# Kernel tuning notes

Measured on AMD Instinct MI355X. Metric: run time of the kernel, lower is better.

Reference implementation:

```python
import jax, jax.numpy as jnp
import numpy as np
import math

NUM_FREQS = 16  # module init num_freqs


def posenc(x, nf):
    # x [..., D] -> [..., D*2*nf]
    freqs = 2.0 ** jnp.arange(nf, dtype=x.dtype)
    xf = x[..., None] * freqs  # [..., D, nf]
    enc = jnp.concatenate([jnp.sin(xf), jnp.cos(xf)], axis=-1)  # [..., D, 2nf]
    return enc.reshape(x.shape[:-1] + (x.shape[-1] * 2 * nf,))


def plucker(rays):
    # rays [..., 6] = [origin, direction] -> [d_norm, cross(o, d_norm)]
    o, dv = rays[..., :3], rays[..., 3:]
    dn = dv / (jnp.linalg.norm(dv, axis=-1, keepdims=True) + 1e-8)
    return jnp.concatenate([dn, jnp.cross(o, dn)], axis=-1)


def grid_sample_bilinear(img, grid):
    # img [N,C,H,W], grid [N,Hg,Wg,2] in [-1,1], align_corners=True, zeros padding
    N, C, H, W = img.shape
    x = (grid[..., 0] + 1.0) * 0.5 * (W - 1)
    y = (grid[..., 1] + 1.0) * 0.5 * (H - 1)
    x0 = jnp.floor(x); x1 = x0 + 1.0
    y0 = jnp.floor(y); y1 = y0 + 1.0
    wx1 = x - x0; wx0 = 1.0 - wx1
    wy1 = y - y0; wy0 = 1.0 - wy1

    def gather(ix, iy):
        valid = ((ix >= 0) & (ix <= W - 1) & (iy >= 0) & (iy <= H - 1)).astype(img.dtype)
        ixc = jnp.clip(ix, 0, W - 1).astype(jnp.int32)
        iyc = jnp.clip(iy, 0, H - 1).astype(jnp.int32)
        vals = jax.vmap(lambda im, iyn, ixn: im[:, iyn, ixn])(img, iyc, ixc)  # [N,C,Hg,Wg]
        return vals * valid[:, None]

    return (gather(x0, y0) * (wx0 * wy0)[:, None]
            + gather(x1, y0) * (wx1 * wy0)[:, None]
            + gather(x0, y1) * (wx0 * wy1)[:, None]
            + gather(x1, y1) * (wx1 * wy1)[:, None])


def _forward(xref, mask_ref, ray_points, rays, R, T, focal, W1, b1, W2, b2, Wv, bv, Wd):
    F = NUM_FREQS
    b, n, hw, c = xref.shape
    d = ray_points.shape[3]
    res = int(math.sqrt(hw))
    # mask (already at res x res; nearest resize is identity)
    xref = xref * mask_ref.reshape(b, n, hw, 1)
    # project sample points into all n+1 camera NDC frames
    pts = ray_points[:, 0]  # [b,hw,d,3]
    p_view = jnp.einsum('bhdk,bvkj->bvhdj', pts, R) + T[:, :, None, None]  # [b,n+1,hw,d,3]
    ndc = focal[:, :, None, None, None] * p_view[..., :2] / p_view[..., 2:3]
    grid = jax.lax.stop_gradient(jnp.clip(jnp.nan_to_num(-ndc[:, 1:]), -1.2, 1.2))
    grid = grid.reshape(b * n, hw, d, 2)
    img = xref.reshape(b * n, res, res, c).transpose(0, 3, 1, 2)  # [(bn),c,res,res]
    pf = grid_sample_bilinear(img, grid)  # [(bn),c,hw,d]
    plane_features = pf.reshape(b, n, c, hw, d).transpose(0, 1, 3, 4, 2)  # [b,n,hw,d,c]

    xyz_iv = p_view                       # view-space points [b,n+1,hw,d,3]
    xyz_iv_enc = posenc(xyz_iv, F)        # [b,n+1,hw,d,6F]

    # target rays (view 0) expressed in every view frame
    o_t, d_t = rays[:, 0, :, :3], rays[:, 0, :, 3:]
    o_iv = jnp.einsum('bhk,bvkj->bvhj', o_t, R) + T[:, :, None]
    d_iv = jnp.einsum('bhk,bvkj->bvhj', d_t, R)
    cam_iv = jnp.concatenate([o_iv, d_iv], -1)[:, 1:]  # [b,n,hw,6]
    cam_iv = jnp.broadcast_to(cam_iv[:, :, :, None, :], (b, n, hw, d, 6))
    cam_iv_enc = posenc(plucker(cam_iv), F // 2)  # [b,n,hw,d,6F]

    xyz_grid = jnp.broadcast_to(xyz_iv_enc[:, :1], (b, n, hw, d, xyz_iv_enc.shape[-1]))
    # reference-view ray origins in target frame
    o_r = rays[:, 1:, :, :3]
    o_tg = jnp.einsum('bnhk,bkj->bnhj', o_r, R[:, 0]) + T[:, 0][:, None, None]
    cam_feat = jnp.broadcast_to(o_tg[:, :, :, None, :], (b, n, hw, d, 3))
    cam_feat_enc = posenc(cam_feat, F)

    plane_in = jnp.concatenate([plane_features, xyz_iv_enc[:, 1:], xyz_iv[:, 1:],
                                cam_iv_enc, cam_iv[..., 3:]], axis=-1)  # [b,n,hw,d,326]
    h = jax.nn.silu(plane_in @ W1 + b1)
    pf_final = h @ W2 + b2  # [b,n,hw,d,C]

    attn_in = jnp.concatenate([plane_features, xyz_grid,
                               jnp.broadcast_to(xyz_iv[:, :1], (b, n, hw, d, 3)),
                               cam_feat, cam_feat_enc], axis=-1)  # [b,n,hw,d,326]
    attn = jax.nn.softmax(attn_in @ Wv + bv, axis=1)  # softmax over views
    fused = (pf_final * attn).sum(1)  # [b,hw,d,C]
    out = fused @ Wd  # decoder (no bias) -> [b,hw,d,1]
    return jnp.concatenate([fused, out], axis=-1), attn


def setup_inputs() -> dict:
    B, N, RES, D, C = 1, 4, 32, 32, 128
    HW = RES * RES
    IN_DIM = C + NUM_FREQS * 3 * 4 + 6  # 326
    key = jax.random.key(0)
    ks = jax.random.split(key, 16)
    xref = jax.random.normal(ks[0], (B, N, HW, C), jnp.float32)
    mask_ref = (jax.random.uniform(ks[1], (B, N, RES, RES)) > 0.1).astype(jnp.float32)
    ray_points = jax.random.uniform(ks[2], (B, 1, HW, D, 3), minval=-0.5, maxval=0.5)
    o = jax.random.uniform(ks[3], (B, N + 1, HW, 3), minval=-0.2, maxval=0.2)
    dirs = jax.random.normal(ks[4], (B, N + 1, HW, 3))
    dirs = dirs / jnp.linalg.norm(dirs, axis=-1, keepdims=True)
    rays = jnp.concatenate([o, dirs], -1)
    R = jnp.linalg.qr(jax.random.normal(ks[5], (B, N + 1, 3, 3)))[0]
    T = jnp.concatenate([jax.random.uniform(ks[6], (B, N + 1, 2), minval=-0.2, maxval=0.2),
                         jax.random.uniform(ks[7], (B, N + 1, 1), minval=2.0, maxval=2.5)], -1)
    focal = jax.random.uniform(ks[8], (B, N + 1), minval=0.8, maxval=1.2)
    W1 = jax.random.normal(ks[9], (IN_DIM, C)) / np.sqrt(IN_DIM)
    b1 = jnp.zeros((C,), jnp.float32)
    W2 = jax.random.normal(ks[10], (C, C)) / np.sqrt(C)
    b2 = jnp.zeros((C,), jnp.float32)
    Wv = jax.random.normal(ks[11], (IN_DIM, 1)) / np.sqrt(IN_DIM)
    bv = jnp.zeros((1,), jnp.float32)
    Wd = jax.random.normal(ks[12], (C, 1)) * 0.01  # zero_module in source; small random for meaningful baseline
    return {"xref": xref, "mask_ref": mask_ref, "ray_points": ray_points, "rays": rays,
            "R": R, "T": T, "focal": focal, "W1": W1, "b1": b1, "W2": W2, "b2": b2,
            "Wv": Wv, "bv": bv, "Wd": Wd}


def reference(xref, mask_ref, ray_points, rays, R, T, focal, W1, b1, W2, b2, Wv, bv, Wd):
    return _forward(xref, mask_ref, ray_points, rays, R, T, focal, W1, b1, W2, b2, Wv, bv, Wd)
```

## Files before the change

### kernel.cpp

```cpp
#include <hip/hip_runtime.h>
#include <hip/hip_bf16.h>
#include <math.h>

#define XH 1024
#define XD 32
#define XC 128
#define XK 326

typedef __attribute__((ext_vector_type(8))) short bf16x8;
typedef __attribute__((ext_vector_type(4))) float f32x4;

__device__ __forceinline__ unsigned short f2b(float f) {
  unsigned u = __float_as_uint(f);
  return (unsigned short)((u + 0x7FFFu + ((u >> 16) & 1u)) >> 16);
}
__device__ __forceinline__ float b2f(unsigned short b) {
  return __uint_as_float(((unsigned)b) << 16);
}
__device__ __forceinline__ unsigned pk2bf(float v0, float v1) {
  __hip_bfloat162 h = __float22bfloat162_rn(make_float2(v0, v1));
  return *reinterpret_cast<unsigned*>(&h);
}

#define WT1 (12 * 8 * 64)
#define WT2 (4 * 8 * 64)

__global__ void prep_frags(const float* __restrict__ W1,
                           const float* __restrict__ W2,
                           unsigned int* __restrict__ ws) {
  int f = blockIdx.x * 256 + threadIdx.x;
  if (f >= WT1 + WT2) return;
  const float* W; int KMAX; int fl; size_t hoff, loff;
  if (f < WT1) { W = W1; KMAX = XK; fl = f; hoff = 0; loff = WT1; }
  else { W = W2; KMAX = XC; fl = f - WT1; hoff = 2 * (size_t)WT1; loff = 2 * (size_t)WT1 + WT2; }
  int l = fl & 63, ct = (fl >> 6) & 7, kc = fl >> 9;
  int c = ct * 16 + (l & 15);
  int kbase = kc * 32 + 8 * (l >> 4);
  unsigned hi[4], lo[4];
  #pragma unroll
  for (int jj = 0; jj < 4; ++jj) {
    int k0 = kbase + 2 * jj;
    float w0 = (k0     < KMAX) ? W[k0 * XC + c]       : 0.f;
    float w1 = (k0 + 1 < KMAX) ? W[(k0 + 1) * XC + c] : 0.f;
    unsigned short h0 = f2b(w0); unsigned short l0 = f2b(w0 - b2f(h0));
    unsigned short h1 = f2b(w1); unsigned short l1 = f2b(w1 - b2f(h1));
    hi[jj] = (unsigned)h0 | ((unsigned)h1 << 16);
    lo[jj] = (unsigned)l0 | ((unsigned)l1 << 16);
  }
  uint4 vh; vh.x = hi[0]; vh.y = hi[1]; vh.z = hi[2]; vh.w = hi[3];
  uint4 vl; vl.x = lo[0]; vl.y = lo[1]; vl.z = lo[2]; vl.w = lo[3];
  *(uint4*)(ws + (hoff + fl) * 4) = vh;
  *(uint4*)(ws + (loff + fl) * 4) = vl;
}


__global__ __launch_bounds__(512, 4)
void nerf_main(const float* __restrict__ xref,
               const float* __restrict__ mask,
               const float* __restrict__ rpts,
               const float* __restrict__ rays,
               const float* __restrict__ Rm,
               const float* __restrict__ Tm,
               const float* __restrict__ focp,
               const float* __restrict__ b1p,
               const float* __restrict__ b2p,
               const float* __restrict__ Wvp,
               const float* __restrict__ bvp,
               const float* __restrict__ Wdp,
               const bf16x8* __restrict__ wfrag,
               float* __restrict__ out0,
               float* __restrict__ out1)
{
  const int h = blockIdx.x;
  const int tid = threadIdx.x;

  __shared__ float sR[5][3][3];
  __shared__ float sT[5][3];
  __shared__ float sFoc[5];
  __shared__ float sRay[5][6];
  __shared__ float sOiv[5][3];
  __shared__ float sDiv[5][3];
  __shared__ float sPlk[4][6];
  __shared__ float sOtg[4][3];
  __shared__ float sPv[5][32][3];
  __shared__ float sBc[4][32][4];
  __shared__ int   sBp[4][32][4];
  __shared__ float sWv[XK];
  __shared__ float sAt[32];
  __shared__ float sBt[4];
  __shared__ float sLogit[4][32];
  __shared__ float sAw[4][32];
  __shared__ float sOutPart[4][32];
  __shared__ __align__(16) unsigned short sEnc2[4][128];
  __shared__ __align__(16) unsigned char uMem[65536];
  unsigned short* sFcHi = (unsigned short*)uMem;
  unsigned short* sFcLo = (unsigned short*)(uMem + 32768);
  unsigned short* sHbHi = (unsigned short*)(uMem + 32768);
  unsigned short* sHbLo = sHbHi + 32 * 128;
  float*          sOut  = (float*)uMem;

  for (int i = tid; i < 45; i += 512) ((float*)sR)[i] = Rm[i];
  for (int i = tid; i < 15; i += 512) ((float*)sT)[i] = Tm[i];
  for (int i = tid; i < 5;  i += 512) sFoc[i] = focp[i];
  for (int i = tid; i < 30; i += 512) { int v = i / 6, j = i % 6; sRay[v][j] = rays[(v*XH + h)*6 + j]; }
  for (int i = tid; i < XK; i += 512) sWv[i] = Wvp[i];
  __syncthreads();

  if (tid < 160) {
    int v = tid >> 5, d = tid & 31;
    float p0 = rpts[(h*XD + d)*3 + 0];
    float p1 = rpts[(h*XD + d)*3 + 1];
    float p2 = rpts[(h*XD + d)*3 + 2];
    #pragma unroll
    for (int j = 0; j < 3; ++j)
      sPv[v][d][j] = p0*sR[v][0][j] + p1*sR[v][1][j] + p2*sR[v][2][j] + sT[v][j];
  } else if (tid < 165) {
    int v = tid - 160;
    #pragma unroll
    for (int j = 0; j < 3; ++j) {
      sOiv[v][j] = sRay[0][0]*sR[v][0][j] + sRay[0][1]*sR[v][1][j] + sRay[0][2]*sR[v][2][j] + sT[v][j];
      sDiv[v][j] = sRay[0][3]*sR[v][0][j] + sRay[0][4]*sR[v][1][j] + sRay[0][5]*sR[v][2][j];
    }
  }
  __syncthreads();

  if (tid < 4) {
    int n = tid;
    float d0 = sDiv[n+1][0], d1 = sDiv[n+1][1], d2 = sDiv[n+1][2];
    float inv = 1.f / (sqrtf(d0*d0 + d1*d1 + d2*d2) + 1e-8f);
    float n0 = d0*inv, n1 = d1*inv, n2 = d2*inv;
    float o0 = sOiv[n+1][0], o1 = sOiv[n+1][1], o2 = sOiv[n+1][2];
    sPlk[n][0] = n0; sPlk[n][1] = n1; sPlk[n][2] = n2;
    sPlk[n][3] = o1*n2 - o2*n1;
    sPlk[n][4] = o2*n0 - o0*n2;
    sPlk[n][5] = o0*n1 - o1*n0;
    #pragma unroll
    for (int j = 0; j < 3; ++j)
      sOtg[n][j] = sRay[1+n][0]*sR[0][0][j] + sRay[1+n][1]*sR[0][1][j] + sRay[1+n][2]*sR[0][2][j] + sT[0][j];
  }
  if (tid >= 32 && tid < 160) {
    int idx = tid - 32, n = idx >> 5, d = idx & 31, v = n + 1;
    float px = sPv[v][d][0], py = sPv[v][d][1], pz = sPv[v][d][2], fo = sFoc[v];
    float gx = -(fo*px)/pz, gy = -(fo*py)/pz;
    if (isnan(gx)) gx = 0.f;
    if (isnan(gy)) gy = 0.f;
    gx = fminf(fmaxf(gx, -1.2f), 1.2f);
    gy = fminf(fmaxf(gy, -1.2f), 1.2f);
    float x = (gx + 1.f)*15.5f, y = (gy + 1.f)*15.5f;
    float x0f = floorf(x), y0f = floorf(y);
    float wx1 = x - x0f, wx0 = 1.f - wx1;
    float wy1 = y - y0f, wy0 = 1.f - wy1;
    int x0i = (int)x0f, y0i = (int)y0f;
    bool vx0 = (x0f >=  0.f) & (x0f <= 31.f);
    bool vx1 = (x0f >= -1.f) & (x0f <= 30.f);
    bool vy0 = (y0f >=  0.f) & (y0f <= 31.f);
    bool vy1 = (y0f >= -1.f) & (y0f <= 30.f);
    int x0c = min(max(x0i, 0), 31), x1c = min(max(x0i + 1, 0), 31);
    int y0c = min(max(y0i, 0), 31), y1c = min(max(y0i + 1, 0), 31);
    int p00 = y0c*32 + x0c, p10 = y0c*32 + x1c, p01 = y1c*32 + x0c, p11 = y1c*32 + x1c;
    sBc[n][d][0] = wx0*wy0*((vx0 && vy0) ? mask[n*XH + p00] : 0.f);
    sBc[n][d][1] = wx1*wy0*((vx1 && vy0) ? mask[n*XH + p10] : 0.f);
    sBc[n][d][2] = wx0*wy1*((vx0 && vy1) ? mask[n*XH + p01] : 0.f);
    sBc[n][d][3] = wx1*wy1*((vx1 && vy1) ? mask[n*XH + p11] : 0.f);
    sBp[n][d][0] = p00; sBp[n][d][1] = p10; sBp[n][d][2] = p01; sBp[n][d][3] = p11;
  }
  if (tid >= 256) {
    int t = tid - 256;
    int d = t >> 3, sub = t & 7;
    float p = 0.f;
    for (int kk = sub * 12; kk < sub * 12 + 12; ++kk) {
      int comp = kk >> 5, idx = kk & 31;
      float ang = sPv[0][d][comp] * (float)(1 << (idx & 15));
      float ev = (idx < 16) ? __sinf(ang) : __cosf(ang);
      p += ev * sWv[128 + kk];
    }
    if (sub == 0)
      for (int j = 0; j < 3; ++j) p += sPv[0][d][j] * sWv[224 + j];
    #pragma unroll
    for (int o = 1; o < 8; o <<= 1) p += __shfl_xor(p, o);
    if (sub == 0) sAt[d] = p;
  }
  __syncthreads();

  {
    int n = tid >> 7, off = tid & 127;
    float val = 0.f;
    if (off >= 3 && off < 99) {
      int kk = off - 3;
      int comp = kk >> 4, idx = kk & 15;
      float ang = sPlk[n][comp] * (float)(1 << (idx & 7));
      val = (idx < 8) ? __sinf(ang) : __cosf(ang);
    } else if (off >= 99 && off < 102) {
      val = sDiv[n + 1][off - 99];
    }
    sEnc2[n][off] = f2b(val);
  }
  if (tid >= 256 && tid < 288) {
    int t = tid - 256, n = t >> 3, sub = t & 7;
    float p = 0.f;
    for (int kk = sub * 12; kk < sub * 12 + 12; ++kk) {
      int comp = kk >> 5, idx = kk & 31;
      float ang = sOtg[n][comp] * (float)(1 << (idx & 15));
      float ev = (idx < 16) ? __sinf(ang) : __cosf(ang);
      p += ev * sWv[230 + kk];
    }
    if (sub == 0) {
      for (int j = 0; j < 3; ++j) p += sOtg[n][j] * sWv[227 + j];
      p += bvp[0];
    }
    #pragma unroll
    for (int o = 1; o < 8; o <<= 1) p += __shfl_xor(p, o);
    if (sub == 0) sBt[n] = p;
  }
  __syncthreads();

  const int brow = tid >> 2;
  const int bn = brow & 3, bd = brow >> 2;
  const int kloc0 = (tid & 3) * 16;
  float plog = 0.f;

  {
    const float* bc = sBc[bn][bd];
    const int*   bp = sBp[bn][bd];
    const float* xb = xref + bn * XH * XC;
    #pragma unroll
    for (int chunk = 0; chunk < 2; ++chunk) {
      int kg = chunk * 64 + kloc0;
      float vv[16];
      #pragma unroll
      for (int q = 0; q < 4; ++q) {
        float4 a0 = *(const float4*)(xb + bp[0] * XC + kg + 4 * q);
        float4 a1 = *(const float4*)(xb + bp[1] * XC + kg + 4 * q);
        float4 a2 = *(const float4*)(xb + bp[2] * XC + kg + 4 * q);
        float4 a3 = *(const float4*)(xb + bp[3] * XC + kg + 4 * q);
        #pragma unroll
        for (int j = 0; j < 4; ++j)
          vv[4 * q + j] = bc[0]*(&a0.x)[j] + bc[1]*(&a1.x)[j]
                        + bc[2]*(&a2.x)[j] + bc[3]*(&a3.x)[j];
      }
      #pragma unroll
      for (int j = 0; j < 16; ++j) plog += vv[j] * sWv[kg + j];
      #pragma unroll
      for (int q = 0; q < 2; ++q) {
        unsigned ph[4], pl[4];
        #pragma unroll
        for (int j = 0; j < 4; ++j) {
          float v0 = vv[8 * q + 2 * j], v1 = vv[8 * q + 2 * j + 1];
          unsigned hp = pk2bf(v0, v1);
          float r0 = v0 - b2f((unsigned short)(hp & 0xFFFF));
          float r1 = v1 - b2f((unsigned short)(hp >> 16));
          ph[j] = hp;
          pl[j] = pk2bf(r0, r1);
        }
        int gidx = (brow * 128 + kg + 8 * q) ^ ((brow & 7) << 3);
        *(uint4*)&sFcHi[gidx] = *(uint4*)ph;
        *(uint4*)&sFcLo[gidx] = *(uint4*)pl;
      }
    }
    {
      float p = plog;
      p += __shfl_xor(p, 1);
      p += __shfl_xor(p, 2);
      if ((tid & 3) == 0) sLogit[bn][bd] = p;
    }
  }
  __syncthreads();

  if (tid < 32) {
    int d = tid;
    float l0 = sLogit[0][d] + sAt[d] + sBt[0];
    float l1 = sLogit[1][d] + sAt[d] + sBt[1];
    float l2 = sLogit[2][d] + sAt[d] + sBt[2];
    float l3 = sLogit[3][d] + sAt[d] + sBt[3];
    float m = fmaxf(fmaxf(l0, l1), fmaxf(l2, l3));
    float e0 = __expf(l0 - m), e1 = __expf(l1 - m), e2 = __expf(l2 - m), e3 = __expf(l3 - m);
    float inv = 1.f / (e0 + e1 + e2 + e3);
    float w0 = e0*inv, w1 = e1*inv, w2 = e2*inv, w3 = e3*inv;
    sAw[0][d] = w0; sAw[1][d] = w1; sAw[2][d] = w2; sAw[3][d] = w3;
    out1[(0*XH + h)*XD + d] = w0;
    out1[(1*XH + h)*XD + d] = w1;
    out1[(2*XH + h)*XD + d] = w2;
    out1[(3*XH + h)*XD + d] = w3;
  }

  const int w = tid >> 6, lane = tid & 63;
  const int rt = w & 3, cg = w >> 2;
  const int lrow = lane & 15, lg = lane >> 4;
  float bias1[4];
  #pragma unroll
  for (int ct = 0; ct < 4; ++ct) bias1[ct] = b1p[cg * 64 + ct * 16 + lrow];

  f32x4 acc1[2][4];
  #pragma unroll
  for (int rf = 0; rf < 2; ++rf)
    #pragma unroll
    for (int ct = 0; ct < 4; ++ct) acc1[rf][ct] = (f32x4){0.f, 0.f, 0.f, 0.f};

  #pragma unroll
  for (int sk = 0; sk < 4; ++sk) {
    const int r0 = rt * 32 + lrow;
    const int ai0 = (r0 * 128 + sk * 32 + 8 * lg) ^ ((r0 & 7) << 3);
    const int ai1 = ai0 + 16 * 128;
    bf16x8 ah0 = *(const bf16x8*)&sFcHi[ai0];
    bf16x8 ah1 = *(const bf16x8*)&sFcHi[ai1];
    bf16x8 al0 = *(const bf16x8*)&sFcLo[ai0];
    bf16x8 al1 = *(const bf16x8*)&sFcLo[ai1];
    const bf16x8* wkh = wfrag + (sk * 8 + cg * 4) * 64 + lane;
    const bf16x8* wkl = wkh + WT1;
    #pragma unroll
    for (int ct = 0; ct < 4; ++ct) {
      bf16x8 bh = wkh[ct * 64];
      bf16x8 bl = wkl[ct * 64];
      acc1[0][ct] = __builtin_amdgcn_mfma_f32_16x16x32_bf16(ah0, bh, acc1[0][ct], 0, 0, 0);
      acc1[0][ct] = __builtin_amdgcn_mfma_f32_16x16x32_bf16(ah0, bl, acc1[0][ct], 0, 0, 0);
      acc1[0][ct] = __builtin_amdgcn_mfma_f32_16x16x32_bf16(al0, bh, acc1[0][ct], 0, 0, 0);
      acc1[1][ct] = __builtin_amdgcn_mfma_f32_16x16x32_bf16(ah1, bh, acc1[1][ct], 0, 0, 0);
      acc1[1][ct] = __builtin_amdgcn_mfma_f32_16x16x32_bf16(ah1, bl, acc1[1][ct], 0, 0, 0);
      acc1[1][ct] = __builtin_amdgcn_mfma_f32_16x16x32_bf16(al1, bh, acc1[1][ct], 0, 0, 0);
    }
  }

  {
    const int r0c = rt * 32 + lrow;
    const int nn = r0c & 3;
    const int dd = r0c >> 2;
    const float* pv0 = sPv[nn + 1][dd];
    const float* pv1 = sPv[nn + 1][dd + 4];
    const unsigned short* enc = sEnc2[nn];
    const float m0 = (lg & 1) ? 256.f : 1.f;
    const bool usn = (lg < 2);

    auto mfma4 = [&](int kc, bf16x8 A0, bf16x8 A1) {
      const bf16x8* wkh = wfrag + (kc * 8 + cg * 4) * 64 + lane;
      const bf16x8* wkl = wkh + WT1;
      #pragma unroll
      for (int ct = 0; ct < 4; ++ct) {
        bf16x8 bh = wkh[ct * 64];
        bf16x8 bl = wkl[ct * 64];
        acc1[0][ct] = __builtin_amdgcn_mfma_f32_16x16x32_bf16(A0, bh, acc1[0][ct], 0, 0, 0);
        acc1[0][ct] = __builtin_amdgcn_mfma_f32_16x16x32_bf16(A0, bl, acc1[0][ct], 0, 0, 0);
        acc1[1][ct] = __builtin_amdgcn_mfma_f32_16x16x32_bf16(A1, bh, acc1[1][ct], 0, 0, 0);
        acc1[1][ct] = __builtin_amdgcn_mfma_f32_16x16x32_bf16(A1, bl, acc1[1][ct], 0, 0, 0);
      }
    };
    auto trigf = [&](const float* pv, int comp) -> bf16x8 {
      float pA = pv[comp] * m0;
      unsigned ph[4];
      #pragma unroll
      for (int mj = 0; mj < 4; ++mj) {
        float a0f = pA * (float)(1 << (2 * mj));
        float a1f = pA * (float)(1 << (2 * mj + 1));
        float v0 = usn ? __sinf(a0f) : __cosf(a0f);
        float v1 = usn ? __sinf(a1f) : __cosf(a1f);
        ph[mj] = pk2bf(v0, v1);
      }
      union { unsigned u[4]; bf16x8 f; } cv;
      cv.u[0] = ph[0]; cv.u[1] = ph[1]; cv.u[2] = ph[2]; cv.u[3] = ph[3];
      return cv.f;
    };
    auto encf = [&](int off) -> bf16x8 {
      return *(const bf16x8*)&enc[off + lg * 8];
    };

    mfma4(4, trigf(pv0, 0), trigf(pv1, 0));
    mfma4(5, trigf(pv0, 1), trigf(pv1, 1));
    mfma4(6, trigf(pv0, 2), trigf(pv1, 2));
    {
      bf16x8 e0 = encf(0);
      bf16x8 e1 = e0;
      if (lg == 0) {
        e0[0] = (short)f2b(pv0[0]); e0[1] = (short)f2b(pv0[1]); e0[2] = (short)f2b(pv0[2]);
        e1[0] = (short)f2b(pv1[0]); e1[1] = (short)f2b(pv1[1]); e1[2] = (short)f2b(pv1[2]);
      }
      mfma4(7, e0, e1);
    }
    { bf16x8 e = encf(32); mfma4(8, e, e); }
    { bf16x8 e = encf(64); mfma4(9, e, e); }
    { bf16x8 e = encf(96); mfma4(10, e, e); }
  }
  __syncthreads();

  #pragma unroll
  for (int rf = 0; rf < 2; ++rf) {
    int d = (rt * 2 + rf) * 4 + lg;
    float a0 = sAw[0][d], a1 = sAw[1][d], a2 = sAw[2][d], a3 = sAw[3][d];
    #pragma unroll
    for (int ct = 0; ct < 4; ++ct) {
      int c = cg * 64 + ct * 16 + lrow;
      float x0 = acc1[rf][ct][0] + bias1[ct];
      float x1 = acc1[rf][ct][1] + bias1[ct];
      float x2 = acc1[rf][ct][2] + bias1[ct];
      float x3 = acc1[rf][ct][3] + bias1[ct];
      float hb = a0 * __fdividef(x0, 1.f + __expf(-x0))
               + a1 * __fdividef(x1, 1.f + __expf(-x1))
               + a2 * __fdividef(x2, 1.f + __expf(-x2))
               + a3 * __fdividef(x3, 1.f + __expf(-x3));
      unsigned short hh = f2b(hb);
      unsigned short hl = f2b(hb - b2f(hh));
      int idx = (d * 128 + c) ^ ((d & 7) << 3);
      sHbHi[idx] = hh; sHbLo[idx] = hl;
    }
  }
  __syncthreads();

  const int rt2 = w & 1, cg2 = w >> 1;
  float bias2[2], wdv[2];
  #pragma unroll
  for (int cti = 0; cti < 2; ++cti) {
    int c = cg2 * 32 + cti * 16 + lrow;
    bias2[cti] = b2p[c]; wdv[cti] = Wdp[c];
  }
  f32x4 acc2[2];
  acc2[0] = (f32x4){0.f, 0.f, 0.f, 0.f};
  acc2[1] = (f32x4){0.f, 0.f, 0.f, 0.f};
  {
    const int ar = rt2 * 16 + lrow;
    #pragma unroll
    for (int kc = 0; kc < 4; ++kc) {
      int aidx = (ar * 128 + kc * 32 + 8 * lg) ^ ((ar & 7) << 3);
      bf16x8 ah = *(const bf16x8*)&sHbHi[aidx];
      bf16x8 al = *(const bf16x8*)&sHbLo[aidx];
      const bf16x8* wkh = wfrag + 2 * WT1 + (kc * 8 + cg2 * 2) * 64 + lane;
      const bf16x8* wkl = wkh + WT2;
      #pragma unroll
      for (int cti = 0; cti < 2; ++cti) {
        bf16x8 bh = wkh[cti * 64];
        bf16x8 bl = wkl[cti * 64];
        acc2[cti] = __builtin_amdgcn_mfma_f32_16x16x32_bf16(ah, bh, acc2[cti], 0, 0, 0);
        acc2[cti] = __builtin_amdgcn_mfma_f32_16x16x32_bf16(ah, bl, acc2[cti], 0, 0, 0);
        acc2[cti] = __builtin_amdgcn_mfma_f32_16x16x32_bf16(al, bh, acc2[cti], 0, 0, 0);
      }
    }
  }

  {
    float part[4] = {0.f, 0.f, 0.f, 0.f};
    #pragma unroll
    for (int cti = 0; cti < 2; ++cti) {
      int c = cg2 * 32 + cti * 16 + lrow;
      #pragma unroll
      for (int i = 0; i < 4; ++i) {
        int d = rt2 * 16 + lg * 4 + i;
        float fv = acc2[cti][i] + bias2[cti];
        sOut[d * 129 + c] = fv;
        part[i] += fv * wdv[cti];
      }
    }
    #pragma unroll
    for (int i = 0; i < 4; ++i) {
      float p = part[i];
      #pragma unroll
      for (int o = 1; o < 16; o <<= 1) p += __shfl_xor(p, o);
      if (lrow == 0) sOutPart[cg2][rt2 * 16 + lg * 4 + i] = p;
    }
  }
  __syncthreads();
  if (tid < 32)
    sOut[tid * 129 + 128] =
      sOutPart[0][tid] + sOutPart[1][tid] + sOutPart[2][tid] + sOutPart[3][tid];
  __syncthreads();
  {
    const float4* src = (const float4*)sOut;
    float4* dst = (float4*)(out0 + (size_t)h * (XD * 129));
    for (int i = tid; i < (XD * 129) / 4; i += 512) dst[i] = src[i];
  }
}

extern "C" void kernel_launch(void* const* d_in, const int* in_sizes, int n_in,
                              void* d_out, int out_size, void* d_ws, size_t ws_size,
                              hipStream_t stream) {
  const float* xref = (const float*)d_in[0];
  const float* mask = (const float*)d_in[1];
  const float* rpts = (const float*)d_in[2];
  const float* rays = (const float*)d_in[3];
  const float* Rm   = (const float*)d_in[4];
  const float* Tm   = (const float*)d_in[5];
  const float* foc  = (const float*)d_in[6];
  const float* W1   = (const float*)d_in[7];
  const float* b1   = (const float*)d_in[8];
  const float* W2   = (const float*)d_in[9];
  const float* b2   = (const float*)d_in[10];
  const float* Wv   = (const float*)d_in[11];
  const float* bv   = (const float*)d_in[12];
  const float* Wd   = (const float*)d_in[13];
  float* out0 = (float*)d_out;
  float* out1 = out0 + (size_t)XH * XD * 129;

  hipLaunchKernelGGL(prep_frags, dim3(32), dim3(256), 0, stream,
                     W1, W2, (unsigned int*)d_ws);
  hipLaunchKernelGGL(nerf_main, dim3(XH), dim3(512), 0, stream,
                     xref, mask, rpts, rays, Rm, Tm, foc,
                     b1, b2, Wv, bv, Wd, (const bf16x8*)d_ws, out0, out1);
}
```

Baseline: 71.63 us.

## Split each ray across two 256-thread blocks handling 16 depth samples each

The main kernel now launches twice as many blocks of 256 threads, each processing half of the 32 depth samples for one ray. Shared memory use per block roughly halves and the MFMA tiling is reorganised so each wave owns 16 rows and all 128 output columns. The aim is better occupancy and finer load balancing across CUs. In exchange, per-ray setup work (camera transforms, Plucker encodings, target attention terms) is duplicated in both blocks, and each wave reads the full weight fragment set.

```diff
diff --git a/kernel.cpp b/kernel.cpp
--- a/kernel.cpp
+++ b/kernel.cpp
@@ -54,7 +54,7 @@
 }
 
 
-__global__ __launch_bounds__(512, 4)
+__global__ __launch_bounds__(256, 4)
 void nerf_main(const float* __restrict__ xref,
                const float* __restrict__ mask,
                const float* __restrict__ rpts,
@@ -71,7 +71,8 @@
                float* __restrict__ out0,
                float* __restrict__ out1)
 {
-  const int h = blockIdx.x;
+  const int h = blockIdx.x >> 1;
+  const int q = blockIdx.x & 1;
   const int tid = threadIdx.x;
 
   __shared__ float sR[5][3][3];
@@ -82,40 +83,40 @@
   __shared__ float sDiv[5][3];
   __shared__ float sPlk[4][6];
   __shared__ float sOtg[4][3];
-  __shared__ float sPv[5][32][3];
-  __shared__ float sBc[4][32][4];
-  __shared__ int   sBp[4][32][4];
+  __shared__ float sPv[5][16][3];
+  __shared__ float sBc[4][16][4];
+  __shared__ int   sBp[4][16][4];
   __shared__ float sWv[XK];
-  __shared__ float sAt[32];
+  __shared__ float sAt[16];
   __shared__ float sBt[4];
-  __shared__ float sLogit[4][32];
-  __shared__ float sAw[4][32];
-  __shared__ float sOutPart[4][32];
+  __shared__ float sLogit[4][16];
+  __shared__ float sAw[4][16];
+  __shared__ float sOutPart[4][16];
   __shared__ __align__(16) unsigned short sEnc2[4][128];
-  __shared__ __align__(16) unsigned char uMem[65536];
+  __shared__ __align__(16) unsigned char uMem[32768];
   unsigned short* sFcHi = (unsigned short*)uMem;
-  unsigned short* sFcLo = (unsigned short*)(uMem + 32768);
-  unsigned short* sHbHi = (unsigned short*)(uMem + 32768);
-  unsigned short* sHbLo = sHbHi + 32 * 128;
+  unsigned short* sFcLo = (unsigned short*)(uMem + 16384);
+  unsigned short* sHbHi = (unsigned short*)(uMem + 16384);
+  unsigned short* sHbLo = sHbHi + 16 * 128;
   float*          sOut  = (float*)uMem;
 
-  for (int i = tid; i < 45; i += 512) ((float*)sR)[i] = Rm[i];
-  for (int i = tid; i < 15; i += 512) ((float*)sT)[i] = Tm[i];
-  for (int i = tid; i < 5;  i += 512) sFoc[i] = focp[i];
-  for (int i = tid; i < 30; i += 512) { int v = i / 6, j = i % 6; sRay[v][j] = rays[(v*XH + h)*6 + j]; }
-  for (int i = tid; i < XK; i += 512) sWv[i] = Wvp[i];
-  __syncthreads();
-
-  if (tid < 160) {
-    int v = tid >> 5, d = tid & 31;
+  for (int i = tid; i < 45; i += 256) ((float*)sR)[i] = Rm[i];
+  for (int i = tid; i < 15; i += 256) ((float*)sT)[i] = Tm[i];
+  for (int i = tid; i < 5;  i += 256) sFoc[i] = focp[i];
+  for (int i = tid; i < 30; i += 256) { int v = i / 6, j = i % 6; sRay[v][j] = rays[(v*XH + h)*6 + j]; }
+  for (int i = tid; i < XK; i += 256) sWv[i] = Wvp[i];
+  __syncthreads();
+
+  if (tid < 80) {
+    int v = tid >> 4, ld = tid & 15, d = q * 16 + ld;
     float p0 = rpts[(h*XD + d)*3 + 0];
     float p1 = rpts[(h*XD + d)*3 + 1];
     float p2 = rpts[(h*XD + d)*3 + 2];
     #pragma unroll
     for (int j = 0; j < 3; ++j)
-      sPv[v][d][j] = p0*sR[v][0][j] + p1*sR[v][1][j] + p2*sR[v][2][j] + sT[v][j];
-  } else if (tid < 165) {
-    int v = tid - 160;
+      sPv[v][ld][j] = p0*sR[v][0][j] + p1*sR[v][1][j] + p2*sR[v][2][j] + sT[v][j];
+  } else if (tid < 85) {
+    int v = tid - 80;
     #pragma unroll
     for (int j = 0; j < 3; ++j) {
       sOiv[v][j] = sRay[0][0]*sR[v][0][j] + sRay[0][1]*sR[v][1][j] + sRay[0][2]*sR[v][2][j] + sT[v][j];
@@ -138,9 +139,9 @@
     for (int j = 0; j < 3; ++j)
       sOtg[n][j] = sRay[1+n][0]*sR[0][0][j] + sRay[1+n][1]*sR[0][1][j] + sRay[1+n][2]*sR[0][2][j] + sT[0][j];
   }
-  if (tid >= 32 && tid < 160) {
-    int idx = tid - 32, n = idx >> 5, d = idx & 31, v = n + 1;
-    float px = sPv[v][d][0], py = sPv[v][d][1], pz = sPv[v][d][2], fo = sFoc[v];
+  if (tid >= 32 && tid < 96) {
+    int idx = tid - 32, n = idx >> 4, ld = idx & 15, v = n + 1;
+    float px = sPv[v][ld][0], py = sPv[v][ld][1], pz = sPv[v][ld][2], fo = sFoc[v];
     float gx = -(fo*px)/pz, gy = -(fo*py)/pz;
     if (isnan(gx)) gx = 0.f;
     if (isnan(gy)) gy = 0.f;
@@ -158,32 +159,32 @@
     int x0c = min(max(x0i, 0), 31), x1c = min(max(x0i + 1, 0), 31);
     int y0c = min(max(y0i, 0), 31), y1c = min(max(y0i + 1, 0), 31);
     int p00 = y0c*32 + x0c, p10 = y0c*32 + x1c, p01 = y1c*32 + x0c, p11 = y1c*32 + x1c;
-    sBc[n][d][0] = wx0*wy0*((vx0 && vy0) ? mask[n*XH + p00] : 0.f);
-    sBc[n][d][1] = wx1*wy0*((vx1 && vy0) ? mask[n*XH + p10] : 0.f);
-    sBc[n][d][2] = wx0*wy1*((vx0 && vy1) ? mask[n*XH + p01] : 0.f);
-    sBc[n][d][3] = wx1*wy1*((vx1 && vy1) ? mask[n*XH + p11] : 0.f);
-    sBp[n][d][0] = p00; sBp[n][d][1] = p10; sBp[n][d][2] = p01; sBp[n][d][3] = p11;
-  }
-  if (tid >= 256) {
-    int t = tid - 256;
-    int d = t >> 3, sub = t & 7;
+    sBc[n][ld][0] = wx0*wy0*((vx0 && vy0) ? mask[n*XH + p00] : 0.f);
+    sBc[n][ld][1] = wx1*wy0*((vx1 && vy0) ? mask[n*XH + p10] : 0.f);
+    sBc[n][ld][2] = wx0*wy1*((vx0 && vy1) ? mask[n*XH + p01] : 0.f);
+    sBc[n][ld][3] = wx1*wy1*((vx1 && vy1) ? mask[n*XH + p11] : 0.f);
+    sBp[n][ld][0] = p00; sBp[n][ld][1] = p10; sBp[n][ld][2] = p01; sBp[n][ld][3] = p11;
+  }
+  if (tid >= 128) {
+    int t = tid - 128;
+    int ld = t >> 3, sub = t & 7;
     float p = 0.f;
     for (int kk = sub * 12; kk < sub * 12 + 12; ++kk) {
       int comp = kk >> 5, idx = kk & 31;
-      float ang = sPv[0][d][comp] * (float)(1 << (idx & 15));
+      float ang = sPv[0][ld][comp] * (float)(1 << (idx & 15));
       float ev = (idx < 16) ? __sinf(ang) : __cosf(ang);
       p += ev * sWv[128 + kk];
     }
     if (sub == 0)
-      for (int j = 0; j < 3; ++j) p += sPv[0][d][j] * sWv[224 + j];
+      for (int j = 0; j < 3; ++j) p += sPv[0][ld][j] * sWv[224 + j];
     #pragma unroll
     for (int o = 1; o < 8; o <<= 1) p += __shfl_xor(p, o);
-    if (sub == 0) sAt[d] = p;
-  }
-  __syncthreads();
-
-  {
-    int n = tid >> 7, off = tid & 127;
+    if (sub == 0) sAt[ld] = p;
+  }
+  __syncthreads();
+
+  for (int s = tid; s < 512; s += 256) {
+    int n = s >> 7, off = s & 127;
     float val = 0.f;
     if (off >= 3 && off < 99) {
       int kk = off - 3;
@@ -195,8 +196,8 @@
     }
     sEnc2[n][off] = f2b(val);
   }
-  if (tid >= 256 && tid < 288) {
-    int t = tid - 256, n = t >> 3, sub = t & 7;
+  if (tid >= 224) {
+    int t = tid - 224, n = t >> 3, sub = t & 7;
     float p = 0.f;
     for (int kk = sub * 12; kk < sub * 12 + 12; ++kk) {
       int comp = kk >> 5, idx = kk & 31;
@@ -215,44 +216,44 @@
   __syncthreads();
 
   const int brow = tid >> 2;
-  const int bn = brow & 3, bd = brow >> 2;
+  const int bn = brow & 3, bld = brow >> 2;
   const int kloc0 = (tid & 3) * 16;
   float plog = 0.f;
 
   {
-    const float* bc = sBc[bn][bd];
-    const int*   bp = sBp[bn][bd];
+    const float* bc = sBc[bn][bld];
+    const int*   bp = sBp[bn][bld];
     const float* xb = xref + bn * XH * XC;
     #pragma unroll
     for (int chunk = 0; chunk < 2; ++chunk) {
       int kg = chunk * 64 + kloc0;
       float vv[16];
       #pragma unroll
-      for (int q = 0; q < 4; ++q) {
-        float4 a0 = *(const float4*)(xb + bp[0] * XC + kg + 4 * q);
-        float4 a1 = *(const float4*)(xb + bp[1] * XC + kg + 4 * q);
-        float4 a2 = *(const float4*)(xb + bp[2] * XC + kg + 4 * q);
-        float4 a3 = *(const float4*)(xb + bp[3] * XC + kg + 4 * q);
+      for (int qq = 0; qq < 4; ++qq) {
+        float4 a0 = *(const float4*)(xb + bp[0] * XC + kg + 4 * qq);
+        float4 a1 = *(const float4*)(xb + bp[1] * XC + kg + 4 * qq);
+        float4 a2 = *(const float4*)(xb + bp[2] * XC + kg + 4 * qq);
+        float4 a3 = *(const float4*)(xb + bp[3] * XC + kg + 4 * qq);
         #pragma unroll
         for (int j = 0; j < 4; ++j)
-          vv[4 * q + j] = bc[0]*(&a0.x)[j] + bc[1]*(&a1.x)[j]
-                        + bc[2]*(&a2.x)[j] + bc[3]*(&a3.x)[j];
+          vv[4 * qq + j] = bc[0]*(&a0.x)[j] + bc[1]*(&a1.x)[j]
+                         + bc[2]*(&a2.x)[j] + bc[3]*(&a3.x)[j];
       }
       #pragma unroll
       for (int j = 0; j < 16; ++j) plog += vv[j] * sWv[kg + j];
       #pragma unroll
-      for (int q = 0; q < 2; ++q) {
+      for (int qq = 0; qq < 2; ++qq) {
         unsigned ph[4], pl[4];
         #pragma unroll
         for (int j = 0; j < 4; ++j) {
-          float v0 = vv[8 * q + 2 * j], v1 = vv[8 * q + 2 * j + 1];
+          float v0 = vv[8 * qq + 2 * j], v1 = vv[8 * qq + 2 * j + 1];
           unsigned hp = pk2bf(v0, v1);
           float r0 = v0 - b2f((unsigned short)(hp & 0xFFFF));
           float r1 = v1 - b2f((unsigned short)(hp >> 16));
           ph[j] = hp;
           pl[j] = pk2bf(r0, r1);
         }
-        int gidx = (brow * 128 + kg + 8 * q) ^ ((brow & 7) << 3);
+        int gidx = (brow * 128 + kg + 8 * qq) ^ ((brow & 7) << 3);
         *(uint4*)&sFcHi[gidx] = *(uint4*)ph;
         *(uint4*)&sFcLo[gidx] = *(uint4*)pl;
       }
@@ -261,22 +262,22 @@
       float p = plog;
       p += __shfl_xor(p, 1);
       p += __shfl_xor(p, 2);
-      if ((tid & 3) == 0) sLogit[bn][bd] = p;
-    }
-  }
-  __syncthreads();
-
-  if (tid < 32) {
-    int d = tid;
-    float l0 = sLogit[0][d] + sAt[d] + sBt[0];
-    float l1 = sLogit[1][d] + sAt[d] + sBt[1];
-    float l2 = sLogit[2][d] + sAt[d] + sBt[2];
-    float l3 = sLogit[3][d] + sAt[d] + sBt[3];
+      if ((tid & 3) == 0) sLogit[bn][bld] = p;
+    }
+  }
+  __syncthreads();
+
+  if (tid < 16) {
+    int ld = tid, d = q * 16 + ld;
+    float l0 = sLogit[0][ld] + sAt[ld] + sBt[0];
+    float l1 = sLogit[1][ld] + sAt[ld] + sBt[1];
+    float l2 = sLogit[2][ld] + sAt[ld] + sBt[2];
+    float l3 = sLogit[3][ld] + sAt[ld] + sBt[3];
     float m = fmaxf(fmaxf(l0, l1), fmaxf(l2, l3));
     float e0 = __expf(l0 - m), e1 = __expf(l1 - m), e2 = __expf(l2 - m), e3 = __expf(l3 - m);
     float inv = 1.f / (e0 + e1 + e2 + e3);
     float w0 = e0*inv, w1 = e1*inv, w2 = e2*inv, w3 = e3*inv;
-    sAw[0][d] = w0; sAw[1][d] = w1; sAw[2][d] = w2; sAw[3][d] = w3;
+    sAw[0][ld] = w0; sAw[1][ld] = w1; sAw[2][ld] = w2; sAw[3][ld] = w3;
     out1[(0*XH + h)*XD + d] = w0;
     out1[(1*XH + h)*XD + d] = w1;
     out1[(2*XH + h)*XD + d] = w2;
@@ -284,63 +285,49 @@
   }
 
   const int w = tid >> 6, lane = tid & 63;
-  const int rt = w & 3, cg = w >> 2;
   const int lrow = lane & 15, lg = lane >> 4;
-  float bias1[4];
+  float bias1[8];
   #pragma unroll
-  for (int ct = 0; ct < 4; ++ct) bias1[ct] = b1p[cg * 64 + ct * 16 + lrow];
-
-  f32x4 acc1[2][4];
+  for (int ct = 0; ct < 8; ++ct) bias1[ct] = b1p[ct * 16 + lrow];
+
+  f32x4 acc1[8];
   #pragma unroll
-  for (int rf = 0; rf < 2; ++rf)
-    #pragma unroll
-    for (int ct = 0; ct < 4; ++ct) acc1[rf][ct] = (f32x4){0.f, 0.f, 0.f, 0.f};
+  for (int ct = 0; ct < 8; ++ct) acc1[ct] = (f32x4){0.f, 0.f, 0.f, 0.f};
 
   #pragma unroll
   for (int sk = 0; sk < 4; ++sk) {
-    const int r0 = rt * 32 + lrow;
+    const int r0 = w * 16 + lrow;
     const int ai0 = (r0 * 128 + sk * 32 + 8 * lg) ^ ((r0 & 7) << 3);
-    const int ai1 = ai0 + 16 * 128;
-    bf16x8 ah0 = *(const bf16x8*)&sFcHi[ai0];
-    bf16x8 ah1 = *(const bf16x8*)&sFcHi[ai1];
-    bf16x8 al0 = *(const bf16x8*)&sFcLo[ai0];
-    bf16x8 al1 = *(const bf16x8*)&sFcLo[ai1];
-    const bf16x8* wkh = wfrag + (sk * 8 + cg * 4) * 64 + lane;
-    const bf16x8* wkl = wkh + WT1;
-    #pragma unroll
-    for (int ct = 0; ct < 4; ++ct) {
-      bf16x8 bh = wkh[ct * 64];
-      bf16x8 bl = wkl[ct * 64];
-      acc1[0][ct] = __builtin_amdgcn_mfma_f32_16x16x32_bf16(ah0, bh, acc1[0][ct], 0, 0, 0);
-      acc1[0][ct] = __builtin_amdgcn_mfma_f32_16x16x32_bf16(ah0, bl, acc1[0][ct], 0, 0, 0);
-      acc1[0][ct] = __builtin_amdgcn_mfma_f32_16x16x32_bf16(al0, bh, acc1[0][ct], 0, 0, 0);
-      acc1[1][ct] = __builtin_amdgcn_mfma_f32_16x16x32_bf16(ah1, bh, acc1[1][ct], 0, 0, 0);
-      acc1[1][ct] = __builtin_amdgcn_mfma_f32_16x16x32_bf16(ah1, bl, acc1[1][ct], 0, 0, 0);
-      acc1[1][ct] = __builtin_amdgcn_mfma_f32_16x16x32_bf16(al1, bh, acc1[1][ct], 0, 0, 0);
-    }
-  }
-
-  {
-    const int r0c = rt * 32 + lrow;
+    bf16x8 ah = *(const bf16x8*)&sFcHi[ai0];
+    bf16x8 al = *(const bf16x8*)&sFcLo[ai0];
+    const bf16x8* wk = wfrag + (sk * 8) * 64 + lane;
+    #pragma unroll
+    for (int ct = 0; ct < 8; ++ct) {
+      bf16x8 bh = wk[ct * 64];
+      bf16x8 bl = wk[WT1 + ct * 64];
+      acc1[ct] = __builtin_amdgcn_mfma_f32_16x16x32_bf16(ah, bh, acc1[ct], 0, 0, 0);
+      acc1[ct] = __builtin_amdgcn_mfma_f32_16x16x32_bf16(ah, bl, acc1[ct], 0, 0, 0);
+      acc1[ct] = __builtin_amdgcn_mfma_f32_16x16x32_bf16(al, bh, acc1[ct], 0, 0, 0);
+    }
+  }
+
+  {
+    const int r0c = w * 16 + lrow;
     const int nn = r0c & 3;
     const int dd = r0c >> 2;
     const float* pv0 = sPv[nn + 1][dd];
-    const float* pv1 = sPv[nn + 1][dd + 4];
     const unsigned short* enc = sEnc2[nn];
     const float m0 = (lg & 1) ? 256.f : 1.f;
     const bool usn = (lg < 2);
 
-    auto mfma4 = [&](int kc, bf16x8 A0, bf16x8 A1) {
-      const bf16x8* wkh = wfrag + (kc * 8 + cg * 4) * 64 + lane;
-      const bf16x8* wkl = wkh + WT1;
-      #pragma unroll
-      for (int ct = 0; ct < 4; ++ct) {
-        bf16x8 bh = wkh[ct * 64];
-        bf16x8 bl = wkl[ct * 64];
-        acc1[0][ct] = __builtin_amdgcn_mfma_f32_16x16x32_bf16(A0, bh, acc1[0][ct], 0, 0, 0);
-        acc1[0][ct] = __builtin_amdgcn_mfma_f32_16x16x32_bf16(A0, bl, acc1[0][ct], 0, 0, 0);
-        acc1[1][ct] = __builtin_amdgcn_mfma_f32_16x16x32_bf16(A1, bh, acc1[1][ct], 0, 0, 0);
-        acc1[1][ct] = __builtin_amdgcn_mfma_f32_16x16x32_bf16(A1, bl, acc1[1][ct], 0, 0, 0);
+    auto mfmaB = [&](int kc, bf16x8 A0) {
+      const bf16x8* wk = wfrag + (kc * 8) * 64 + lane;
+      #pragma unroll
+      for (int ct = 0; ct < 8; ++ct) {
+        bf16x8 bh = wk[ct * 64];
+        bf16x8 bl = wk[WT1 + ct * 64];
+        acc1[ct] = __builtin_amdgcn_mfma_f32_16x16x32_bf16(A0, bh, acc1[ct], 0, 0, 0);
+        acc1[ct] = __builtin_amdgcn_mfma_f32_16x16x32_bf16(A0, bl, acc1[ct], 0, 0, 0);
       }
     };
     auto trigf = [&](const float* pv, int comp) -> bf16x8 {
@@ -362,70 +349,65 @@
       return *(const bf16x8*)&enc[off + lg * 8];
     };
 
-    mfma4(4, trigf(pv0, 0), trigf(pv1, 0));
-    mfma4(5, trigf(pv0, 1), trigf(pv1, 1));
-    mfma4(6, trigf(pv0, 2), trigf(pv1, 2));
+    mfmaB(4, trigf(pv0, 0));
+    mfmaB(5, trigf(pv0, 1));
+    mfmaB(6, trigf(pv0, 2));
     {
       bf16x8 e0 = encf(0);
-      bf16x8 e1 = e0;
       if (lg == 0) {
         e0[0] = (short)f2b(pv0[0]); e0[1] = (short)f2b(pv0[1]); e0[2] = (short)f2b(pv0[2]);
-        e1[0] = (short)f2b(pv1[0]); e1[1] = (short)f2b(pv1[1]); e1[2] = (short)f2b(pv1[2]);
-      }
-      mfma4(7, e0, e1);
-    }
-    { bf16x8 e = encf(32); mfma4(8, e, e); }
-    { bf16x8 e = encf(64); mfma4(9, e, e); }
-    { bf16x8 e = encf(96); mfma4(10, e, e); }
-  }
-  __syncthreads();
-
-  #pragma unroll
-  for (int rf = 0; rf < 2; ++rf) {
-    int d = (rt * 2 + rf) * 4 + lg;
-    float a0 = sAw[0][d], a1 = sAw[1][d], a2 = sAw[2][d], a3 = sAw[3][d];
-    #pragma unroll
-    for (int ct = 0; ct < 4; ++ct) {
-      int c = cg * 64 + ct * 16 + lrow;
-      float x0 = acc1[rf][ct][0] + bias1[ct];
-      float x1 = acc1[rf][ct][1] + bias1[ct];
-      float x2 = acc1[rf][ct][2] + bias1[ct];
-      float x3 = acc1[rf][ct][3] + bias1[ct];
+      }
+      mfmaB(7, e0);
+    }
+    mfmaB(8, encf(32));
+    mfmaB(9, encf(64));
+    mfmaB(10, encf(96));
+  }
+  __syncthreads();
+
+  {
+    int ld = w * 4 + lg;
+    float a0 = sAw[0][ld], a1 = sAw[1][ld], a2 = sAw[2][ld], a3 = sAw[3][ld];
+    #pragma unroll
+    for (int ct = 0; ct < 8; ++ct) {
+      int c = ct * 16 + lrow;
+      float x0 = acc1[ct][0] + bias1[ct];
+      float x1 = acc1[ct][1] + bias1[ct];
+      float x2 = acc1[ct][2] + bias1[ct];
+      float x3 = acc1[ct][3] + bias1[ct];
       float hb = a0 * __fdividef(x0, 1.f + __expf(-x0))
                + a1 * __fdividef(x1, 1.f + __expf(-x1))
                + a2 * __fdividef(x2, 1.f + __expf(-x2))
                + a3 * __fdividef(x3, 1.f + __expf(-x3));
       unsigned short hh = f2b(hb);
       unsigned short hl = f2b(hb - b2f(hh));
-      int idx = (d * 128 + c) ^ ((d & 7) << 3);
+      int idx = (ld * 128 + c) ^ ((ld & 7) << 3);
       sHbHi[idx] = hh; sHbLo[idx] = hl;
     }
   }
   __syncthreads();
 
-  const int rt2 = w & 1, cg2 = w >> 1;
   float bias2[2], wdv[2];
   #pragma unroll
   for (int cti = 0; cti < 2; ++cti) {
-    int c = cg2 * 32 + cti * 16 + lrow;
+    int c = w * 32 + cti * 16 + lrow;
     bias2[cti] = b2p[c]; wdv[cti] = Wdp[c];
   }
   f32x4 acc2[2];
   acc2[0] = (f32x4){0.f, 0.f, 0.f, 0.f};
   acc2[1] = (f32x4){0.f, 0.f, 0.f, 0.f};
   {
-    const int ar = rt2 * 16 + lrow;
+    const int ar = lrow;
     #pragma unroll
     for (int kc = 0; kc < 4; ++kc) {
       int aidx = (ar * 128 + kc * 32 + 8 * lg) ^ ((ar & 7) << 3);
       bf16x8 ah = *(const bf16x8*)&sHbHi[aidx];
       bf16x8 al = *(const bf16x8*)&sHbLo[aidx];
-      const bf16x8* wkh = wfrag + 2 * WT1 + (kc * 8 + cg2 * 2) * 64 + lane;
-      const bf16x8* wkl = wkh + WT2;
+      const bf16x8* wk = wfrag + 2 * WT1 + (kc * 8 + w * 2) * 64 + lane;
       #pragma unroll
       for (int cti = 0; cti < 2; ++cti) {
-        bf16x8 bh = wkh[cti * 64];
-        bf16x8 bl = wkl[cti * 64];
+        bf16x8 bh = wk[cti * 64];
+        bf16x8 bl = wk[WT2 + cti * 64];
         acc2[cti] = __builtin_amdgcn_mfma_f32_16x16x32_bf16(ah, bh, acc2[cti], 0, 0, 0);
         acc2[cti] = __builtin_amdgcn_mfma_f32_16x16x32_bf16(ah, bl, acc2[cti], 0, 0, 0);
         acc2[cti] = __builtin_amdgcn_mfma_f32_16x16x32_bf16(al, bh, acc2[cti], 0, 0, 0);
@@ -437,12 +419,12 @@
     float part[4] = {0.f, 0.f, 0.f, 0.f};
     #pragma unroll
     for (int cti = 0; cti < 2; ++cti) {
-      int c = cg2 * 32 + cti * 16 + lrow;
+      int c = w * 32 + cti * 16 + lrow;
       #pragma unroll
       for (int i = 0; i < 4; ++i) {
-        int d = rt2 * 16 + lg * 4 + i;
+        int ld = lg * 4 + i;
         float fv = acc2[cti][i] + bias2[cti];
-        sOut[d * 129 + c] = fv;
+        sOut[ld * 129 + c] = fv;
         part[i] += fv * wdv[cti];
       }
     }
@@ -451,18 +433,18 @@
       float p = part[i];
       #pragma unroll
       for (int o = 1; o < 16; o <<= 1) p += __shfl_xor(p, o);
-      if (lrow == 0) sOutPart[cg2][rt2 * 16 + lg * 4 + i] = p;
-    }
-  }
-  __syncthreads();
-  if (tid < 32)
+      if (lrow == 0) sOutPart[w][lg * 4 + i] = p;
+    }
+  }
+  __syncthreads();
+  if (tid < 16)
     sOut[tid * 129 + 128] =
       sOutPart[0][tid] + sOutPart[1][tid] + sOutPart[2][tid] + sOutPart[3][tid];
   __syncthreads();
   {
     const float4* src = (const float4*)sOut;
-    float4* dst = (float4*)(out0 + (size_t)h * (XD * 129));
-    for (int i = tid; i < (XD * 129) / 4; i += 512) dst[i] = src[i];
+    float4* dst = (float4*)(out0 + (size_t)h * (XD * 129) + (size_t)q * (16 * 129));
+    for (int i = tid; i < (16 * 129) / 4; i += 256) dst[i] = src[i];
   }
 }
 
@@ -488,7 +470,7 @@
 
   hipLaunchKernelGGL(prep_frags, dim3(32), dim3(256), 0, stream,
                      W1, W2, (unsigned int*)d_ws);
-  hipLaunchKernelGGL(nerf_main, dim3(XH), dim3(512), 0, stream,
+  hipLaunchKernelGGL(nerf_main, dim3(XH * 2), dim3(256), 0, stream,
                      xref, mask, rpts, rays, Rm, Tm, foc,
                      b1, b2, Wv, bv, Wd, (const bf16x8*)d_ws, out0, out1);
 }
```

Measured after the change: 81.47 us. 13.7% more time.
